# Kernel optimization log

Measured on AMD Instinct MI355X. Metric: run time of the kernel, lower is better.

## Reference

```python
import jax, jax.numpy as jnp
import numpy as np

B, S, HID = 2, 2048, 2048
NH, NKV, HD = 16, 4, 128
MAXPOS = 2048


def _rope_tables(features, length, max_timescale=10000.0):
    fraction = jnp.arange(0, features, 2, dtype=jnp.float32) / features
    inv_freq = 1.0 / (max_timescale ** fraction)
    sinusoid = jnp.einsum('i,j->ij', jnp.arange(length, dtype=jnp.float32), inv_freq)
    sinusoid = jnp.concatenate([sinusoid, sinusoid], axis=-1)  # [length, features]
    return jnp.sin(sinusoid), jnp.cos(sinusoid)


def rotate_half(x):
    x1, x2 = jnp.split(x, 2, axis=-1)
    return jnp.concatenate([-x2, x1], axis=-1)


def setup_inputs() -> dict:
    key = jax.random.key(0)
    k1, k2, k3, k4, k5 = jax.random.split(key, 5)
    scale = 1.0 / np.sqrt(HID)
    hidden_states = jax.random.normal(k1, (B, S, HID), dtype=jnp.float32)
    Wq = jax.random.normal(k2, (NH * HD, HID), dtype=jnp.float32) * scale
    Wk = jax.random.normal(k3, (NKV * HD, HID), dtype=jnp.float32) * scale
    Wv = jax.random.normal(k4, (NKV * HD, HID), dtype=jnp.float32) * scale
    Wo = jax.random.normal(k5, (HID, NH * HD), dtype=jnp.float32) * scale
    # causal additive mask [B,1,S,S]
    neg = jnp.finfo(jnp.float32).min
    causal = jnp.where(jnp.tril(jnp.ones((S, S), dtype=bool)), 0.0, neg)
    attention_mask = jnp.broadcast_to(causal[None, None], (B, 1, S, S))
    sin, cos = _rope_tables(HD, MAXPOS)
    return {"hidden_states": hidden_states, "attention_mask": attention_mask,
            "Wq": Wq, "Wk": Wk, "Wv": Wv, "Wo": Wo, "sin": sin, "cos": cos}


def reference(hidden_states, attention_mask, Wq, Wk, Wv, Wo, sin, cos):
    bsz, qlen, _ = hidden_states.shape
    # projections (Linear, no bias): x @ W.T -> [B,S,heads,hd]
    q = (hidden_states @ Wq.T).reshape(bsz, qlen, NH, HD)
    k = (hidden_states @ Wk.T).reshape(bsz, qlen, NKV, HD)
    v = (hidden_states @ Wv.T).reshape(bsz, qlen, NKV, HD)
    # rotary embedding (applied in [B,S,H,D] layout)
    qcos = cos[:qlen][None, :, None, :]
    qsin = sin[:qlen][None, :, None, :]
    q = q * qcos + rotate_half(q) * qsin
    k = k * qcos + rotate_half(k) * qsin
    # GQA: repeat_kv equivalent via einsum grouping; expand kv heads to NH
    n_rep = NH // NKV
    q_g = q.reshape(bsz, qlen, NKV, n_rep, HD)  # group queries per kv head
    # scores: NOTE original applies no 1/sqrt(d) scaling
    scores = jnp.einsum('bqhrd,bkhd->bhrqk', q_g, k).reshape(bsz, NH, qlen, qlen)
    mask = attention_mask.at[:, :, :, 0].set(0.0)
    scores = scores + mask
    probs = jax.nn.softmax(scores.astype(jnp.float32), axis=-1).astype(q.dtype)
    probs_g = probs.reshape(bsz, NKV, n_rep, qlen, qlen)
    out = jnp.einsum('bhrqk,bkhd->bqhrd', probs_g, v).reshape(bsz, qlen, NH * HD)
    return out @ Wo.T
```

## Files before the change

### kernel.cpp

```cpp
#include <hip/hip_runtime.h>
#include <hip/hip_bf16.h>

typedef _Float16 f16x8 __attribute__((ext_vector_type(8)));
typedef __fp16 h16x2 __attribute__((ext_vector_type(2)));
typedef float f32x4 __attribute__((ext_vector_type(4)));
typedef float f32x16 __attribute__((ext_vector_type(16)));

#define B_    2
#define S_    2048
#define HID_  2048
#define NH_   16
#define NKV_  4
#define HD_   128
#define M_TOK 4096
#define NQKV  3072

#define MFMA16(a, b, c) __builtin_amdgcn_mfma_f32_16x16x32_f16(a, b, c, 0, 0, 0)
#define MFMA32(a, b, c) __builtin_amdgcn_mfma_f32_32x32x16_f16(a, b, c, 0, 0, 0)

union UW { unsigned u; h16x2 h; };

__device__ __forceinline__ unsigned short f2h(float f) {
  _Float16 h = (_Float16)f;
  return *(unsigned short*)&h;
}

__device__ __forceinline__ void gload_lds16(const unsigned short* g, unsigned short* l) {
  __builtin_amdgcn_global_load_lds((const __attribute__((address_space(1))) void*)g,
                                   (__attribute__((address_space(3))) void*)l,
                                   16, 0, 0);
}

__global__ void cast_f32_f16(const float* __restrict__ src, unsigned short* __restrict__ dst, int n4) {
  int i = blockIdx.x * blockDim.x + threadIdx.x;
  int stride = gridDim.x * blockDim.x;
  for (int idx = i; idx < n4; idx += stride) {
    float4 v = reinterpret_cast<const float4*>(src)[idx];
    ushort4 o;
    o.x = f2h(v.x); o.y = f2h(v.y); o.z = f2h(v.z); o.w = f2h(v.w);
    reinterpret_cast<ushort4*>(dst)[idx] = o;
  }
}

#define BM 128
#define BN 128
#define BK 32

__global__ __launch_bounds__(256) void gemm_bt_f16(
    const unsigned short* __restrict__ A, const unsigned short* __restrict__ Bm,
    float* __restrict__ C, int M, int N, int K) {
  __shared__ unsigned short As[BM * BK];
  __shared__ unsigned short Bs[BN * BK];
  const int tid  = threadIdx.x;
  const int lane = tid & 63;
  const int wave = tid >> 6;
  const int nbn  = N / BN;
  const int brow = (blockIdx.x / nbn) * BM;
  const int bcol = (blockIdx.x % nbn) * BN;
  const int wr = (wave >> 1) * 64;
  const int wc = (wave & 1) * 64;

  const int srow = wave * 16 + (lane >> 2);
  const int scol = (lane & 3) * 8;
  const unsigned short* ag = A + (size_t)(brow + srow) * K + scol;
  const unsigned short* bg = Bm + (size_t)(bcol + srow) * K + scol;
  unsigned short* aldsw = As + wave * 512;
  unsigned short* bldsw = Bs + wave * 512;

  f32x4 acc[4][4];
#pragma unroll
  for (int m = 0; m < 4; ++m)
#pragma unroll
    for (int n = 0; n < 4; ++n) acc[m][n] = (f32x4){0.f, 0.f, 0.f, 0.f};

  const int lr = lane & 15;
  const int lg = lane >> 4;

  for (int kt = 0; kt < K; kt += BK) {
    __syncthreads();
    gload_lds16(ag + kt, aldsw);
    gload_lds16(ag + (size_t)64 * K + kt, aldsw + 2048);
    gload_lds16(bg + kt, bldsw);
    gload_lds16(bg + (size_t)64 * K + kt, bldsw + 2048);
    __syncthreads();
    f16x8 af[4], bfr[4];
#pragma unroll
    for (int m = 0; m < 4; ++m)
      af[m] = *reinterpret_cast<const f16x8*>(&As[(wr + m * 16 + lr) * BK + lg * 8]);
#pragma unroll
    for (int n = 0; n < 4; ++n)
      bfr[n] = *reinterpret_cast<const f16x8*>(&Bs[(wc + n * 16 + lr) * BK + lg * 8]);
#pragma unroll
    for (int m = 0; m < 4; ++m)
#pragma unroll
      for (int n = 0; n < 4; ++n)
        acc[m][n] = MFMA16(af[m], bfr[n], acc[m][n]);
  }

#pragma unroll
  for (int m = 0; m < 4; ++m) {
#pragma unroll
    for (int r = 0; r < 4; ++r) {
      int row = brow + wr + m * 16 + lg * 4 + r;
      float* cp = C + (size_t)row * N + bcol + wc + lr;
#pragma unroll
      for (int n = 0; n < 4; ++n) cp[n * 16] = acc[m][n][r];
    }
  }
}

__global__ void rope_relayout(const float* __restrict__ QKV,
                              const float* __restrict__ sin_t, const float* __restrict__ cos_t,
                              unsigned short* __restrict__ Qo, unsigned short* __restrict__ Ko,
                              unsigned short* __restrict__ Vt) {
  int idx = blockIdx.x * blockDim.x + threadIdx.x;
  int d  = idx & 63;
  int t  = idx >> 6;
  int hh = t % 24;
  int bs = t / 24;
  int s  = bs & (S_ - 1);
  int b  = bs >> 11;
  const float* xrow = QKV + (size_t)bs * NQKV;
  if (hh < 16) {
    float x0 = xrow[hh * 128 + d], x1 = xrow[hh * 128 + 64 + d];
    float c = cos_t[s * 128 + d], sn = sin_t[s * 128 + d];
    unsigned short* qp = Qo + (((size_t)(b * 16 + hh) * S_) + s) * 128 + d;
    qp[0]  = f2h(x0 * c - x1 * sn);
    qp[64] = f2h(x1 * c + x0 * sn);
  } else if (hh < 20) {
    int kvh = hh - 16;
    float x0 = xrow[2048 + kvh * 128 + d], x1 = xrow[2048 + kvh * 128 + 64 + d];
    float c = cos_t[s * 128 + d], sn = sin_t[s * 128 + d];
    unsigned short* kp = Ko + (((size_t)(b * 4 + kvh) * S_) + s) * 128 + d;
    kp[0]  = f2h(x0 * c - x1 * sn);
    kp[64] = f2h(x1 * c + x0 * sn);
  } else {
    int kvh = hh - 20;
    float x0 = xrow[2560 + kvh * 128 + d], x1 = xrow[2560 + kvh * 128 + 64 + d];
    unsigned short* vp = Vt + ((size_t)(b * 4 + kvh) * 128 + d) * S_ + s;
    vp[0]        = f2h(x0);
    vp[64 * S_]  = f2h(x1);
  }
}

__global__ __launch_bounds__(256, 2) void flash_attn6(
    const unsigned short* __restrict__ Q, const unsigned short* __restrict__ Kk,
    const unsigned short* __restrict__ Vt, unsigned short* __restrict__ Ao) {
  __shared__ _Float16 Kl[2][64 * 128];
  __shared__ _Float16 Vl[2][128 * 64];
  const int lane = threadIdx.x & 63;
  const int w    = threadIdx.x >> 6;
  const int bh   = blockIdx.x & 31;
  const int bq   = 15 - (int)(blockIdx.x >> 5);
  const int b    = bh >> 4, h = bh & 15, kvh = h >> 2;
  const int q31  = lane & 31;
  const int hi   = lane >> 5;
  const int qb   = bq * 128;
  const int wqb  = qb + w * 32;
  const int qrow = wqb + q31;

  const _Float16* Qp = (const _Float16*)Q + (((size_t)(b * 16 + h) * S_) + qrow) * 128;
  const _Float16* Kp = (const _Float16*)Kk + ((size_t)(b * 4 + kvh) * S_) * 128;
  const _Float16* Vp = (const _Float16*)Vt + ((size_t)(b * 4 + kvh) * 128) * S_;

  f16x8 qf[8];
#pragma unroll
  for (int s = 0; s < 8; ++s) {
    f16x8 t = *reinterpret_cast<const f16x8*>(Qp + s * 16 + hi * 8);
#pragma unroll
    for (int j = 0; j < 8; ++j) t[j] = (_Float16)((float)t[j] * 1.44269504f);
    qf[s] = t;
  }

  f32x16 po0 = {}, po1 = {}, po2 = {}, po3 = {};
  float m = -1e30f, l = 0.f;

  const int krow = (lane >> 4);
  const int vrow = (lane >> 3);
  const int wklim = wqb + 32;
  const int nt = qb / 64 + 2;

#define STAGE(K0S, BUF)                                                               \
  {                                                                                   \
    unsigned short* kdst = (unsigned short*)Kl[BUF] + w * 2048;                       \
    unsigned short* vdst = (unsigned short*)Vl[BUF] + w * 2048;                       \
    _Pragma("unroll") for (int jj = 0; jj < 4; ++jj) {                                \
      const int j = w * 4 + jj;                                                       \
      const int kr = j * 4 + krow;                                                    \
      const int kc = (lane & 15) ^ (kr & 7);                                          \
      gload_lds16((const unsigned short*)(Kp + (size_t)((K0S) + kr) * 128 + kc * 8),  \
                  kdst + jj * 512);                                                   \
      const int vr = j * 8 + vrow;                                                    \
      const int vc = (lane & 7) ^ (vr & 7);                                           \
      gload_lds16((const unsigned short*)(Vp + (size_t)vr * S_ + (K0S) + vc * 8),     \
                  vdst + jj * 512);                                                   \
    }                                                                                 \
  }

  STAGE(0, 0)
  __syncthreads();

  int cur = 0;
  const int r7 = q31 & 7;
  for (int t = 0; t < nt; ++t) {
    const int k0 = t * 64;
    if (t + 1 < nt) STAGE((t + 1) * 64, cur ^ 1)

    if (k0 < wklim) {
      f32x16 s0 = {}, s1 = {};
      const _Float16* Kc = Kl[cur];
      __builtin_amdgcn_s_setprio(1);
#pragma unroll
      for (int s = 0; s < 8; ++s) {
        const int cc = (hi + 2 * s) ^ r7;
        f16x8 kf0 = *reinterpret_cast<const f16x8*>(Kc + q31 * 128 + cc * 8);
        f16x8 kf1 = *reinterpret_cast<const f16x8*>(Kc + (q31 + 32) * 128 + cc * 8);
        s0 = MFMA32(kf0, qf[s], s0);
        s1 = MFMA32(kf1, qf[s], s1);
      }
      __builtin_amdgcn_s_setprio(0);

      if (k0 + 63 > wqb) {
        int qrel = qrow - k0 - 4 * hi;
#pragma unroll
        for (int r = 0; r < 16; ++r) {
          int cr = (r & 3) + 8 * (r >> 2);
          if (cr > qrel)      s0[r] = -1e30f;
          if (cr + 32 > qrel) s1[r] = -1e30f;
        }
      }
      float tmx[8];
#pragma unroll
      for (int r = 0; r < 8; ++r)
        tmx[r] = fmaxf(fmaxf(s0[r], s0[r + 8]), fmaxf(s1[r], s1[r + 8]));
#pragma unroll
      for (int d = 4; d > 0; d >>= 1)
#pragma unroll
        for (int r = 0; r < d; ++r) tmx[r] = fmaxf(tmx[r], tmx[r + d]);
      float pmax = fmaxf(tmx[0], __shfl_xor(tmx[0], 32));
      if (__any(pmax > m + 8.0f)) {
        float mn = fmaxf(m, pmax);
        float sc = __builtin_amdgcn_exp2f(m - mn);
        l *= sc;
#pragma unroll
        for (int r = 0; r < 16; ++r) {
          po0[r] *= sc; po1[r] *= sc; po2[r] *= sc; po3[r] *= sc;
        }
        m = mn;
      }
#pragma unroll
      for (int r = 0; r < 16; ++r) s0[r] = __builtin_amdgcn_exp2f(s0[r] - m);
#pragma unroll
      for (int r = 0; r < 16; ++r) s1[r] = __builtin_amdgcn_exp2f(s1[r] - m);
      float u[8];
#pragma unroll
      for (int r = 0; r < 8; ++r)
        u[r] = (s0[r] + s0[r + 8]) + (s1[r] + s1[r + 8]);
#pragma unroll
      for (int d = 4; d > 0; d >>= 1)
#pragma unroll
        for (int r = 0; r < d; ++r) u[r] += u[r + d];
      l += u[0] + __shfl_xor(u[0], 32);

      f16x8 pa[4];
#pragma unroll
      for (int sl = 0; sl < 4; ++sl) {
        f32x16 sv = (sl < 2) ? s0 : s1;
        const int R = (sl & 1) * 8;
        UW w00, w01, w10, w11;
        w00.h = __builtin_amdgcn_cvt_pkrtz(sv[R + 0], sv[R + 1]);
        w01.h = __builtin_amdgcn_cvt_pkrtz(sv[R + 2], sv[R + 3]);
        w10.h = __builtin_amdgcn_cvt_pkrtz(sv[R + 4], sv[R + 5]);
        w11.h = __builtin_amdgcn_cvt_pkrtz(sv[R + 6], sv[R + 7]);
        unsigned x00 = __shfl_xor(w00.u, 32);
        unsigned x01 = __shfl_xor(w01.u, 32);
        unsigned x10 = __shfl_xor(w10.u, 32);
        unsigned x11 = __shfl_xor(w11.u, 32);
        UW W0, W1, W2, W3;
        W0.u = hi ? x10 : w00.u;
        W1.u = hi ? x11 : w01.u;
        W2.u = hi ? w10.u : x00;
        W3.u = hi ? w11.u : x01;
        union { unsigned uu[4]; f16x8 v; } pk;
        pk.uu[0] = W0.u; pk.uu[1] = W1.u; pk.uu[2] = W2.u; pk.uu[3] = W3.u;
        pa[sl] = pk.v;
      }

      const _Float16* Vc = Vl[cur];
      __builtin_amdgcn_s_setprio(1);
#pragma unroll
      for (int s = 0; s < 4; ++s) {
        const int cc = (hi + 2 * s) ^ r7;
        f16x8 vf0 = *reinterpret_cast<const f16x8*>(Vc + q31 * 64 + cc * 8);
        po0 = MFMA32(vf0, pa[s], po0);
        f16x8 vf1 = *reinterpret_cast<const f16x8*>(Vc + (q31 + 32) * 64 + cc * 8);
        po1 = MFMA32(vf1, pa[s], po1);
        f16x8 vf2 = *reinterpret_cast<const f16x8*>(Vc + (q31 + 64) * 64 + cc * 8);
        po2 = MFMA32(vf2, pa[s], po2);
        f16x8 vf3 = *reinterpret_cast<const f16x8*>(Vc + (q31 + 96) * 64 + cc * 8);
        po3 = MFMA32(vf3, pa[s], po3);
      }
      __builtin_amdgcn_s_setprio(0);
    }

    __syncthreads();
    cur ^= 1;
  }
#undef STAGE

  float inv = 1.0f / l;
  unsigned short* orow = Ao + ((size_t)(b * S_ + qrow)) * 2048 + h * 128;
#define STORE_DB(PO, DB)                                                          \
  {                                                                               \
    _Pragma("unroll") for (int a4 = 0; a4 < 4; ++a4) {                            \
      UW e0, e1;                                                                  \
      e0.h = __builtin_amdgcn_cvt_pkrtz(PO[4 * a4 + 0] * inv, PO[4 * a4 + 1] * inv); \
      e1.h = __builtin_amdgcn_cvt_pkrtz(PO[4 * a4 + 2] * inv, PO[4 * a4 + 3] * inv); \
      unsigned long long pv = ((unsigned long long)e1.u << 32) | e0.u;            \
      *reinterpret_cast<unsigned long long*>(orow + DB * 32 + a4 * 8 + hi * 4) = pv; \
    }                                                                             \
  }
  STORE_DB(po0, 0)
  STORE_DB(po1, 1)
  STORE_DB(po2, 2)
  STORE_DB(po3, 3)
#undef STORE_DB
}

extern "C" void kernel_launch(void* const* d_in, const int* in_sizes, int n_in,
                              void* d_out, int out_size, void* d_ws, size_t ws_size,
                              hipStream_t stream) {
  const float* hs    = (const float*)d_in[0];
  const float* Wq    = (const float*)d_in[2];
  const float* Wk    = (const float*)d_in[3];
  const float* Wv    = (const float*)d_in[4];
  const float* Wo    = (const float*)d_in[5];
  const float* sin_t = (const float*)d_in[6];
  const float* cos_t = (const float*)d_in[7];

  char* ws = (char*)d_ws;
  unsigned short* Xb    = (unsigned short*)ws; ws += (size_t)M_TOK * HID_ * 2;
  unsigned short* Wqkvb = (unsigned short*)ws; ws += (size_t)NQKV * HID_ * 2;
  unsigned short* Wob   = (unsigned short*)ws; ws += (size_t)HID_ * HID_ * 2;
  float*          QKV   = (float*)ws;          ws += (size_t)M_TOK * NQKV * 4;
  unsigned short* Qb    = (unsigned short*)ws; ws += (size_t)B_ * NH_ * S_ * HD_ * 2;
  unsigned short* Kb    = (unsigned short*)ws; ws += (size_t)B_ * NKV_ * S_ * HD_ * 2;
  unsigned short* Vtb   = (unsigned short*)ws; ws += (size_t)B_ * NKV_ * S_ * HD_ * 2;
  unsigned short* Aob   = (unsigned short*)ws; ws += (size_t)M_TOK * HID_ * 2;

  cast_f32_f16<<<2048, 256, 0, stream>>>(hs, Xb, M_TOK * HID_ / 4);
  cast_f32_f16<<<1024, 256, 0, stream>>>(Wq, Wqkvb, 2048 * 2048 / 4);
  cast_f32_f16<<<512,  256, 0, stream>>>(Wk, Wqkvb + 2048 * 2048, 512 * 2048 / 4);
  cast_f32_f16<<<512,  256, 0, stream>>>(Wv, Wqkvb + 2560 * 2048, 512 * 2048 / 4);
  cast_f32_f16<<<1024, 256, 0, stream>>>(Wo, Wob, 2048 * 2048 / 4);

  gemm_bt_f16<<<(M_TOK / BM) * (NQKV / BN), 256, 0, stream>>>(Xb, Wqkvb, QKV, M_TOK, NQKV, HID_);

  rope_relayout<<<(B_ * S_ * 24 * 64) / 256, 256, 0, stream>>>(QKV, sin_t, cos_t, Qb, Kb, Vtb);

  flash_attn6<<<512, 256, 0, stream>>>(Qb, Kb, Vtb, Aob);

  gemm_bt_f16<<<(M_TOK / BM) * (HID_ / BN), 256, 0, stream>>>(Aob, Wob, (float*)d_out, M_TOK, HID_, HID_);
}
```

Measured before the change: 259.2 us.

## Store QKV projection in fp16 and load V fragments directly from global

The QKV GEMM now writes fp16 output instead of fp32. This halves the intermediate's write and read traffic, and rope_relayout copies V without any conversion. The attention kernel drops its V shared-memory staging and loads V fragments straight from global memory into registers at the start of each tile. That removes LDS traffic and halves shared memory use, at the cost of more register pressure and uncoalesced, latency-exposed global loads that are no longer overlapped by the double buffer.

```diff
diff --git a/kernel.cpp b/kernel.cpp
--- a/kernel.cpp
+++ b/kernel.cpp
@@ -46,9 +46,10 @@
 #define BN 128
 #define BK 32
 
+template <bool OUT16>
 __global__ __launch_bounds__(256) void gemm_bt_f16(
     const unsigned short* __restrict__ A, const unsigned short* __restrict__ Bm,
-    float* __restrict__ C, int M, int N, int K) {
+    void* __restrict__ Cv, int M, int N, int K) {
   __shared__ unsigned short As[BM * BK];
   __shared__ unsigned short Bs[BN * BK];
   const int tid  = threadIdx.x;
@@ -102,14 +103,20 @@
 #pragma unroll
     for (int r = 0; r < 4; ++r) {
       int row = brow + wr + m * 16 + lg * 4 + r;
-      float* cp = C + (size_t)row * N + bcol + wc + lr;
-#pragma unroll
-      for (int n = 0; n < 4; ++n) cp[n * 16] = acc[m][n][r];
+      if (OUT16) {
+        unsigned short* cp = (unsigned short*)Cv + (size_t)row * N + bcol + wc + lr;
+#pragma unroll
+        for (int n = 0; n < 4; ++n) cp[n * 16] = f2h(acc[m][n][r]);
+      } else {
+        float* cp = (float*)Cv + (size_t)row * N + bcol + wc + lr;
+#pragma unroll
+        for (int n = 0; n < 4; ++n) cp[n * 16] = acc[m][n][r];
+      }
     }
   }
 }
 
-__global__ void rope_relayout(const float* __restrict__ QKV,
+__global__ void rope_relayout(const unsigned short* __restrict__ QKV,
                               const float* __restrict__ sin_t, const float* __restrict__ cos_t,
                               unsigned short* __restrict__ Qo, unsigned short* __restrict__ Ko,
                               unsigned short* __restrict__ Vt) {
@@ -120,34 +127,34 @@
   int bs = t / 24;
   int s  = bs & (S_ - 1);
   int b  = bs >> 11;
-  const float* xrow = QKV + (size_t)bs * NQKV;
+  const _Float16* xrow = (const _Float16*)QKV + (size_t)bs * NQKV;
   if (hh < 16) {
-    float x0 = xrow[hh * 128 + d], x1 = xrow[hh * 128 + 64 + d];
+    float x0 = (float)xrow[hh * 128 + d], x1 = (float)xrow[hh * 128 + 64 + d];
     float c = cos_t[s * 128 + d], sn = sin_t[s * 128 + d];
     unsigned short* qp = Qo + (((size_t)(b * 16 + hh) * S_) + s) * 128 + d;
     qp[0]  = f2h(x0 * c - x1 * sn);
     qp[64] = f2h(x1 * c + x0 * sn);
   } else if (hh < 20) {
     int kvh = hh - 16;
-    float x0 = xrow[2048 + kvh * 128 + d], x1 = xrow[2048 + kvh * 128 + 64 + d];
+    float x0 = (float)xrow[2048 + kvh * 128 + d], x1 = (float)xrow[2048 + kvh * 128 + 64 + d];
     float c = cos_t[s * 128 + d], sn = sin_t[s * 128 + d];
     unsigned short* kp = Ko + (((size_t)(b * 4 + kvh) * S_) + s) * 128 + d;
     kp[0]  = f2h(x0 * c - x1 * sn);
     kp[64] = f2h(x1 * c + x0 * sn);
   } else {
     int kvh = hh - 20;
-    float x0 = xrow[2560 + kvh * 128 + d], x1 = xrow[2560 + kvh * 128 + 64 + d];
+    unsigned short x0 = QKV[(size_t)bs * NQKV + 2560 + kvh * 128 + d];
+    unsigned short x1 = QKV[(size_t)bs * NQKV + 2560 + kvh * 128 + 64 + d];
     unsigned short* vp = Vt + ((size_t)(b * 4 + kvh) * 128 + d) * S_ + s;
-    vp[0]        = f2h(x0);
-    vp[64 * S_]  = f2h(x1);
-  }
-}
-
-__global__ __launch_bounds__(256, 2) void flash_attn6(
+    vp[0]        = x0;
+    vp[64 * S_]  = x1;
+  }
+}
+
+__global__ __launch_bounds__(256, 2) void flash_attn7(
     const unsigned short* __restrict__ Q, const unsigned short* __restrict__ Kk,
     const unsigned short* __restrict__ Vt, unsigned short* __restrict__ Ao) {
   __shared__ _Float16 Kl[2][64 * 128];
-  __shared__ _Float16 Vl[2][128 * 64];
   const int lane = threadIdx.x & 63;
   const int w    = threadIdx.x >> 6;
   const int bh   = blockIdx.x & 31;
@@ -176,24 +183,18 @@
   float m = -1e30f, l = 0.f;
 
   const int krow = (lane >> 4);
-  const int vrow = (lane >> 3);
   const int wklim = wqb + 32;
   const int nt = qb / 64 + 2;
 
 #define STAGE(K0S, BUF)                                                               \
   {                                                                                   \
     unsigned short* kdst = (unsigned short*)Kl[BUF] + w * 2048;                       \
-    unsigned short* vdst = (unsigned short*)Vl[BUF] + w * 2048;                       \
     _Pragma("unroll") for (int jj = 0; jj < 4; ++jj) {                                \
       const int j = w * 4 + jj;                                                       \
       const int kr = j * 4 + krow;                                                    \
       const int kc = (lane & 15) ^ (kr & 7);                                          \
       gload_lds16((const unsigned short*)(Kp + (size_t)((K0S) + kr) * 128 + kc * 8),  \
                   kdst + jj * 512);                                                   \
-      const int vr = j * 8 + vrow;                                                    \
-      const int vc = (lane & 7) ^ (vr & 7);                                           \
-      gload_lds16((const unsigned short*)(Vp + (size_t)vr * S_ + (K0S) + vc * 8),     \
-                  vdst + jj * 512);                                                   \
     }                                                                                 \
   }
 
@@ -207,6 +208,16 @@
     if (t + 1 < nt) STAGE((t + 1) * 64, cur ^ 1)
 
     if (k0 < wklim) {
+      const _Float16* vb = Vp + (size_t)q31 * S_ + k0 + hi * 8;
+      f16x8 vf[16];
+#pragma unroll
+      for (int s = 0; s < 4; ++s) {
+        vf[s]      = *reinterpret_cast<const f16x8*>(vb + s * 16);
+        vf[4 + s]  = *reinterpret_cast<const f16x8*>(vb + (size_t)32 * S_ + s * 16);
+        vf[8 + s]  = *reinterpret_cast<const f16x8*>(vb + (size_t)64 * S_ + s * 16);
+        vf[12 + s] = *reinterpret_cast<const f16x8*>(vb + (size_t)96 * S_ + s * 16);
+      }
+
       f32x16 s0 = {}, s1 = {};
       const _Float16* Kc = Kl[cur];
       __builtin_amdgcn_s_setprio(1);
@@ -286,19 +297,13 @@
         pa[sl] = pk.v;
       }
 
-      const _Float16* Vc = Vl[cur];
       __builtin_amdgcn_s_setprio(1);
 #pragma unroll
       for (int s = 0; s < 4; ++s) {
-        const int cc = (hi + 2 * s) ^ r7;
-        f16x8 vf0 = *reinterpret_cast<const f16x8*>(Vc + q31 * 64 + cc * 8);
-        po0 = MFMA32(vf0, pa[s], po0);
-        f16x8 vf1 = *reinterpret_cast<const f16x8*>(Vc + (q31 + 32) * 64 + cc * 8);
-        po1 = MFMA32(vf1, pa[s], po1);
-        f16x8 vf2 = *reinterpret_cast<const f16x8*>(Vc + (q31 + 64) * 64 + cc * 8);
-        po2 = MFMA32(vf2, pa[s], po2);
-        f16x8 vf3 = *reinterpret_cast<const f16x8*>(Vc + (q31 + 96) * 64 + cc * 8);
-        po3 = MFMA32(vf3, pa[s], po3);
+        po0 = MFMA32(vf[s], pa[s], po0);
+        po1 = MFMA32(vf[4 + s], pa[s], po1);
+        po2 = MFMA32(vf[8 + s], pa[s], po2);
+        po3 = MFMA32(vf[12 + s], pa[s], po3);
       }
       __builtin_amdgcn_s_setprio(0);
     }
@@ -342,7 +347,7 @@
   unsigned short* Xb    = (unsigned short*)ws; ws += (size_t)M_TOK * HID_ * 2;
   unsigned short* Wqkvb = (unsigned short*)ws; ws += (size_t)NQKV * HID_ * 2;
   unsigned short* Wob   = (unsigned short*)ws; ws += (size_t)HID_ * HID_ * 2;
-  float*          QKV   = (float*)ws;          ws += (size_t)M_TOK * NQKV * 4;
+  unsigned short* QKV   = (unsigned short*)ws; ws += (size_t)M_TOK * NQKV * 2;
   unsigned short* Qb    = (unsigned short*)ws; ws += (size_t)B_ * NH_ * S_ * HD_ * 2;
   unsigned short* Kb    = (unsigned short*)ws; ws += (size_t)B_ * NKV_ * S_ * HD_ * 2;
   unsigned short* Vtb   = (unsigned short*)ws; ws += (size_t)B_ * NKV_ * S_ * HD_ * 2;
@@ -354,11 +359,11 @@
   cast_f32_f16<<<512,  256, 0, stream>>>(Wv, Wqkvb + 2560 * 2048, 512 * 2048 / 4);
   cast_f32_f16<<<1024, 256, 0, stream>>>(Wo, Wob, 2048 * 2048 / 4);
 
-  gemm_bt_f16<<<(M_TOK / BM) * (NQKV / BN), 256, 0, stream>>>(Xb, Wqkvb, QKV, M_TOK, NQKV, HID_);
+  gemm_bt_f16<true><<<(M_TOK / BM) * (NQKV / BN), 256, 0, stream>>>(Xb, Wqkvb, QKV, M_TOK, NQKV, HID_);
 
   rope_relayout<<<(B_ * S_ * 24 * 64) / 256, 256, 0, stream>>>(QKV, sin_t, cos_t, Qb, Kb, Vtb);
 
-  flash_attn6<<<512, 256, 0, stream>>>(Qb, Kb, Vtb, Aob);
-
-  gemm_bt_f16<<<(M_TOK / BM) * (HID_ / BN), 256, 0, stream>>>(Aob, Wob, (float*)d_out, M_TOK, HID_, HID_);
-}
+  flash_attn7<<<512, 256, 0, stream>>>(Qb, Kb, Vtb, Aob);
+
+  gemm_bt_f16<false><<<(M_TOK / BM) * (HID_ / BN), 256, 0, stream>>>(Aob, Wob, d_out, M_TOK, HID_, HID_);
+}
```

After: 283.6 us. 1.09x slower.
